# Optimization experiments

Measured on AMD Instinct MI355X. Metric: run time of the kernel, lower is better.

## Reference

```python
import jax, jax.numpy as jnp
import numpy as np

N = 100000   # nodes
E = 1600000  # edges
G = 256      # graphs in batch
IN = 128     # in_feats
H = 64       # h_feats


def _xavier(k, shape):
    fan_in, fan_out = shape
    lim = float(np.sqrt(6.0 / (fan_in + fan_out)))
    return jax.random.uniform(k, shape, jnp.float32, -lim, lim)


def setup_inputs() -> dict:
    key = jax.random.key(0)
    ks = jax.random.split(key, 12)
    x = jax.random.normal(ks[0], (N, IN), jnp.float32)
    src = jax.random.randint(ks[1], (E,), 0, N)
    dst = jax.random.randint(ks[2], (E,), 0, N)
    ew = jax.random.uniform(ks[3], (E,), jnp.float32)
    gid = jnp.sort(jax.random.randint(ks[4], (N,), 0, G))
    def lin(k, fi, fo):
        kw, kb = jax.random.split(k)
        lim = float(np.sqrt(1.0 / fi))
        return (jax.random.uniform(kw, (fi, fo), jnp.float32, -lim, lim),
                jax.random.uniform(kb, (fo,), jnp.float32, -lim, lim))
    W1 = _xavier(ks[5], (IN, H)); b1 = jnp.zeros((H,), jnp.float32)
    W2 = _xavier(ks[6], (H, H));  b2 = jnp.zeros((H,), jnp.float32)
    W3 = _xavier(ks[7], (H, H));  b3 = jnp.zeros((H,), jnp.float32)
    Dw1, Db1 = lin(ks[8], H, 16)
    Dw2, Db2 = lin(ks[9], 16, 8)
    Dw3, Db3 = lin(ks[10], 8, 1)
    return {"x": x, "src": src, "dst": dst, "ew": ew, "gid": gid,
            "W1": W1, "b1": b1, "W2": W2, "b2": b2, "W3": W3, "b3": b3,
            "Dw1": Dw1, "Db1": Db1, "Dw2": Dw2, "Db2": Db2, "Dw3": Dw3, "Db3": Db3}


def reference(x, src, dst, ew, gid, W1, b1, W2, b2, W3, b3,
              Dw1, Db1, Dw2, Db2, Dw3, Db3):
    n = x.shape[0]
    # DGL GraphConv norm='both': unweighted degrees, clamped to >= 1
    deg_out = jnp.zeros((n,), x.dtype).at[src].add(1.0)
    deg_in = jnp.zeros((n,), x.dtype).at[dst].add(1.0)
    ns = jax.lax.rsqrt(jnp.maximum(deg_out, 1.0))  # src-side norm
    nd = jax.lax.rsqrt(jnp.maximum(deg_in, 1.0))   # dst-side norm

    def conv(h, W, b):
        # apply weight first (in >= out), then gather-scale-scatter
        h = (h * ns[:, None]) @ W                      # [N, out]
        m = h[src] * ew[:, None]                       # [E, out] edge messages
        agg = jnp.zeros((n, W.shape[1]), h.dtype).at[dst].add(m)
        return agg * nd[:, None] + b

    h = jax.nn.relu(conv(x, W1, b1))
    h = jax.nn.relu(conv(h, W2, b2))
    h = jax.nn.relu(conv(h, W3, b3))

    # mean_nodes: per-graph mean pooling
    counts = jnp.zeros((G,), h.dtype).at[gid].add(1.0)
    pooled = jnp.zeros((G, h.shape[1]), h.dtype).at[gid].add(h)
    pooled = pooled / jnp.maximum(counts, 1.0)[:, None]

    h = jax.nn.relu(pooled @ Dw1 + Db1)
    h = jax.nn.relu(h @ Dw2 + Db2)
    return jax.nn.sigmoid(h @ Dw3 + Db3)  # [G, 1]
```

## Files before the change

### kernel.cpp

```cpp
#include <hip/hip_runtime.h>
#include <math.h>

#define N_NODES 100000
#define N_EDGES 1600000
#define G_GRAPHS 256
#define IN_F 128
#define H_F 64

#define HB 20
#define HCHUNK (N_EDGES / HB)
#define NWORDS (N_NODES / 4)
#define HNODES 25000
#define HWORDS (HNODES / 4)
#define HR 4

#define NREG 160
#define REG_NODES 625
#define BUCKET_CAP 11000
#define BSPAN 6400
#define NB_BUCKET (N_EDGES / BSPAN)
#define NQ 4
#define QDIV 25000

typedef unsigned int uint_t;
typedef unsigned short ushort_t;
typedef unsigned char uchar_t;
typedef __attribute__((ext_vector_type(8))) short short8;
typedef __attribute__((ext_vector_type(4))) float floatx4;
typedef __attribute__((ext_vector_type(2))) float floatx2;

__device__ __forceinline__ ushort_t f2bf(float f) {
  uint_t u = __float_as_uint(f);
  uint_t r = (u + 0x7fffu + ((u >> 16) & 1u)) >> 16;
  return (ushort_t)r;
}
__device__ __forceinline__ float bflo(uint_t u) { return __uint_as_float(u << 16); }
__device__ __forceinline__ uchar_t f2fp8(float f) {
  return (uchar_t)(__builtin_amdgcn_cvt_pk_fp8_f32(f, f, 0, false) & 0xff);
}
__device__ __forceinline__ int sw_idx(int row, int kshort) {
  int slot = kshort >> 3;
  return row * 64 + (((slot ^ (row & 7)) << 3) | (kshort & 7));
}

__global__ __launch_bounds__(256) void build_a_kernel(
    const int* __restrict__ src, const int* __restrict__ dst,
    const float* __restrict__ ew, int* __restrict__ bcnt,
    uint2* __restrict__ bucket, uint_t* __restrict__ p8src) {
  __shared__ uint_t shm[BSPAN + 2 * NREG];
  if (blockIdx.x < NB_BUCKET) {
    uint_t* rl = shm;
    int* cnt = (int*)(shm + BSPAN);
    int* cur = cnt + NREG;
    const int e0 = blockIdx.x * BSPAN;

    for (int i = threadIdx.x; i < NREG; i += 256) cnt[i] = 0;
    __syncthreads();

    for (int i = threadIdx.x; i < BSPAN; i += 256) {
      uint_t d = (uint_t)dst[e0 + i];
      uint_t r = d / REG_NODES;
      uint_t loc = d - r * REG_NODES;
      rl[i] = (r << 16) | loc;
      atomicAdd(&cnt[r], 1);
    }
    __syncthreads();

    for (int i = threadIdx.x; i < NREG; i += 256)
      cur[i] = atomicAdd(&bcnt[i], cnt[i]);
    __syncthreads();

    for (int i = threadIdx.x; i < BSPAN; i += 256) {
      uint_t v = rl[i];
      uint_t r = v >> 16, loc = v & 0xffffu;
      int pos = atomicAdd(&cur[r], 1);
      if (pos < BUCKET_CAP)
        bucket[(size_t)r * BUCKET_CAP + pos] = make_uint2(
            (loc << 17) | (uint_t)src[e0 + i], __float_as_uint(ew[e0 + i]));
    }
  } else {
    uint_t* h = shm;
    const int idx = blockIdx.x - NB_BUCKET;
    const int r = idx / HB;
    const int b = idx % HB;
    const uint_t rbase = (uint_t)(r * HNODES);

    for (int i = threadIdx.x; i < HWORDS; i += 256) h[i] = 0u;
    __syncthreads();

    const uint4* k4 = (const uint4*)(src + b * HCHUNK);
    for (int i = threadIdx.x; i < HCHUNK / 4; i += 256) {
      uint4 v = k4[i];
      uint_t t;
      t = v.x - rbase; if (t < (uint_t)HNODES) atomicAdd(&h[t >> 2], 1u << ((t & 3u) * 8u));
      t = v.y - rbase; if (t < (uint_t)HNODES) atomicAdd(&h[t >> 2], 1u << ((t & 3u) * 8u));
      t = v.z - rbase; if (t < (uint_t)HNODES) atomicAdd(&h[t >> 2], 1u << ((t & 3u) * 8u));
      t = v.w - rbase; if (t < (uint_t)HNODES) atomicAdd(&h[t >> 2], 1u << ((t & 3u) * 8u));
    }
    __syncthreads();

    uint_t* outp = p8src + (size_t)b * NWORDS + r * HWORDS;
    for (int i = threadIdx.x; i < HWORDS; i += 256) outp[i] = h[i];
  }
}

__global__ __launch_bounds__(1024) void build_b_kernel(
    const uint2* __restrict__ bucket, const int* __restrict__ bcnt,
    const uint_t* __restrict__ p8src, uint_t* __restrict__ csr,
    int2* __restrict__ rc, float* __restrict__ nd, float* __restrict__ ns) {
  __shared__ uint_t staged[BUCKET_CAP];
  __shared__ int cnt4[REG_NODES * NQ];
  __shared__ int sc4[REG_NODES * NQ];
  __shared__ int ts[1024];
  const int tid = threadIdx.x;
  if (blockIdx.x >= NREG) {
    int w = (blockIdx.x - NREG) * 1024 + tid;
    if (w >= NWORDS) return;
    int c0 = 0, c1 = 0, c2 = 0, c3 = 0;
    for (int b = 0; b < HB; ++b) {
      uint_t xv = p8src[(size_t)b * NWORDS + w];
      c0 += (int)(xv & 0xffu);
      c1 += (int)((xv >> 8) & 0xffu);
      c2 += (int)((xv >> 16) & 0xffu);
      c3 += (int)((xv >> 24) & 0xffu);
    }
    ((float4*)ns)[w] = make_float4(
        rsqrtf(fmaxf((float)c0, 1.0f)), rsqrtf(fmaxf((float)c1, 1.0f)),
        rsqrtf(fmaxf((float)c2, 1.0f)), rsqrtf(fmaxf((float)c3, 1.0f)));
    return;
  }
  const int r = blockIdx.x;
  const int nE = min(bcnt[r], BUCKET_CAP);

  ts[tid] = (tid < NREG) ? min(bcnt[tid], BUCKET_CAP) : 0;
  for (int i = tid; i < REG_NODES * NQ; i += 1024) cnt4[i] = 0;
  __syncthreads();
  for (int off = 1; off < 256; off <<= 1) {
    int t = (tid >= off) ? ts[tid - off] : 0;
    __syncthreads();
    ts[tid] += t;
    __syncthreads();
  }
  const int csr_base = (r == 0) ? 0 : ts[r - 1];
  __syncthreads();

  const uint2* bk = bucket + (size_t)r * BUCKET_CAP;
  for (int i = tid; i < nE; i += 1024) {
    uint_t ex = bk[i].x;
    uint_t loc = ex >> 17;
    uint_t q = (ex & 0x1ffffu) / QDIV;
    atomicAdd(&cnt4[loc * NQ + q], 1);
  }
  __syncthreads();

  int c4[NQ], cv = 0;
  if (tid < REG_NODES) {
#pragma unroll
    for (int q = 0; q < NQ; ++q) { c4[q] = cnt4[tid * NQ + q]; cv += c4[q]; }
  }
  ts[tid] = (tid < REG_NODES) ? cv : 0;
  __syncthreads();
  for (int off = 1; off < 1024; off <<= 1) {
    int t = (tid >= off) ? ts[tid - off] : 0;
    __syncthreads();
    ts[tid] += t;
    __syncthreads();
  }
  if (tid < REG_NODES) {
    int run = (tid == 0) ? 0 : ts[tid - 1];
    int v = r * REG_NODES + tid;
    rc[v] = make_int2(csr_base + run, cv);
    nd[v] = rsqrtf(fmaxf((float)cv, 1.0f));
#pragma unroll
    for (int q = 0; q < NQ; ++q) { sc4[tid * NQ + q] = run; run += c4[q]; }
  }
  __syncthreads();

  for (int i = tid; i < nE; i += 1024) {
    uint2 e = bk[i];
    uint_t loc = e.x >> 17;
    uint_t q = (e.x & 0x1ffffu) / QDIV;
    int pos = atomicAdd(&sc4[loc * NQ + q], 1);
    staged[pos] = ((uint_t)(f2bf(__uint_as_float(e.y)) & 0x7fff) << 17) |
                  (e.x & 0x1ffffu);
  }
  __syncthreads();

  for (int i = tid; i < nE; i += 1024) csr[csr_base + i] = staged[i];
}

template <int K, bool AFP32>
__global__ __launch_bounds__(256) void gemm_mfma_kernel(
    const void* __restrict__ Xin, const float* __restrict__ W,
    const float* __restrict__ ns, uchar_t* __restrict__ T, int ntiles) {
  constexpr int CH = K / 32;
  constexpr int WROW = K + 8;
  __shared__ __align__(16) ushort_t Wt[64 * WROW];
  const int tid = threadIdx.x;

  for (int i = tid; i < K * 64; i += 256) {
    int k = i >> 6, nn = i & 63;
    Wt[nn * WROW + k] = f2bf(W[i]);
  }
  __syncthreads();

  const int wave = tid >> 6;
  const int lane = tid & 63;
  const int tile = blockIdx.x * 4 + wave;
  if (tile >= ntiles) return;
  const int m = lane & 15;
  const int q = lane >> 4;
  const int node0 = tile * 16;

  short8 afrag[CH];
  if (AFP32) {
    const float* xr = (const float*)Xin + (size_t)(node0 + m) * K + q * 8;
#pragma unroll
    for (int c = 0; c < CH; ++c) {
      float4 xa = *(const float4*)(xr + c * 32);
      float4 xb = *(const float4*)(xr + c * 32 + 4);
      short8 a;
      a[0] = (short)f2bf(xa.x); a[1] = (short)f2bf(xa.y);
      a[2] = (short)f2bf(xa.z); a[3] = (short)f2bf(xa.w);
      a[4] = (short)f2bf(xb.x); a[5] = (short)f2bf(xb.y);
      a[6] = (short)f2bf(xb.z); a[7] = (short)f2bf(xb.w);
      afrag[c] = a;
    }
  } else {
    const ushort_t* xr = (const ushort_t*)Xin + (size_t)(node0 + m) * K + q * 8;
#pragma unroll
    for (int c = 0; c < CH; ++c)
      afrag[c] = *(const short8*)(xr + c * 32);
  }

  floatx4 acc[4];
#pragma unroll
  for (int t = 0; t < 4; ++t) acc[t] = (floatx4){0.f, 0.f, 0.f, 0.f};

#pragma unroll
  for (int t = 0; t < 4; ++t) {
    const ushort_t* wr = &Wt[(t * 16 + m) * WROW + q * 8];
#pragma unroll
    for (int c = 0; c < CH; ++c) {
      short8 bfrag = *(const short8*)(wr + c * 32);
      acc[t] = __builtin_amdgcn_mfma_f32_16x16x32_bf16(afrag[c], bfrag, acc[t], 0, 0, 0);
    }
  }

  float4 nsv = *(const float4*)(ns + node0 + q * 4);
  const float nsa[4] = {nsv.x, nsv.y, nsv.z, nsv.w};
#pragma unroll
  for (int t = 0; t < 4; ++t) {
#pragma unroll
    for (int r = 0; r < 4; ++r) {
      int node = node0 + q * 4 + r;
      T[(size_t)node * 64 + t * 16 + m] = f2fp8(acc[t][r] * nsa[r]);
    }
  }
}

__device__ __forceinline__ void gacc1(float acc[8], uint_t e, uint2 p) {
  float w = __uint_as_float((e >> 17) << 16);
  floatx2 a;
  a = __builtin_amdgcn_cvt_pk_f32_fp8(p.x, false);
  acc[0] = fmaf(a.x, w, acc[0]); acc[1] = fmaf(a.y, w, acc[1]);
  a = __builtin_amdgcn_cvt_pk_f32_fp8(p.x, true);
  acc[2] = fmaf(a.x, w, acc[2]); acc[3] = fmaf(a.y, w, acc[3]);
  a = __builtin_amdgcn_cvt_pk_f32_fp8(p.y, false);
  acc[4] = fmaf(a.x, w, acc[4]); acc[5] = fmaf(a.y, w, acc[5]);
  a = __builtin_amdgcn_cvt_pk_f32_fp8(p.y, true);
  acc[6] = fmaf(a.x, w, acc[6]); acc[7] = fmaf(a.y, w, acc[7]);
}

template <bool POOL>
__global__ __launch_bounds__(256, 6) void fused_kernel(
    const uint_t* __restrict__ csr, const int2* __restrict__ rc,
    const uchar_t* __restrict__ T, const float* __restrict__ nd,
    const float* __restrict__ bias, const float* __restrict__ ns,
    const float* __restrict__ W, uchar_t* __restrict__ Tout,
    const int* __restrict__ gid, float* __restrict__ pooled) {
  __shared__ __align__(16) ushort_t Hs[POOL ? 8 : 64 * 64];
  __shared__ __align__(16) ushort_t Wt[POOL ? 8 : 64 * 64];
  __shared__ float gaccF[POOL ? 256 : 1];
  __shared__ int g0s;
  const int tid = threadIdx.x;
  const int node_base = blockIdx.x * 64;
  const int vlast = min(node_base + 63, N_NODES - 1);

  if constexpr (POOL) {
    gaccF[tid] = 0.0f;
    if (tid == 0) g0s = gid[node_base];
  } else {
    for (int i = tid; i < H_F * 64; i += 256) {
      int k = i >> 6, nn = i & 63;
      Wt[sw_idx(nn, k)] = f2bf(W[i]);
    }
  }
  __syncthreads();

  const int lane = tid & 63;
  const int wv = tid >> 6;
  const int o = lane >> 3, l = lane & 7;
  const uint2* Tp = (const uint2*)T;

  const float4 b0 = *(const float4*)&bias[l * 8];
  const float4 b1v = *(const float4*)&bias[l * 8 + 4];

#pragma unroll 1
  for (int pass = 0; pass < 2; ++pass) {
    const int ln = pass * 32 + wv * 8 + o;
    const int v = node_base + ln;
    if (v < N_NODES) {
      int2 rcv = rc[v];
      int k = rcv.x;
      const int ke = rcv.x + rcv.y;
      float acc[8] = {0, 0, 0, 0, 0, 0, 0, 0};

      for (; k + 4 <= ke; k += 4) {
        uint_t e0 = csr[k], e1 = csr[k + 1], e2 = csr[k + 2], e3 = csr[k + 3];
        uint2 p0 = Tp[(size_t)(e0 & 0x1ffffu) * 8 + l];
        uint2 p1 = Tp[(size_t)(e1 & 0x1ffffu) * 8 + l];
        uint2 p2 = Tp[(size_t)(e2 & 0x1ffffu) * 8 + l];
        uint2 p3 = Tp[(size_t)(e3 & 0x1ffffu) * 8 + l];
        gacc1(acc, e0, p0); gacc1(acc, e1, p1);
        gacc1(acc, e2, p2); gacc1(acc, e3, p3);
      }
      for (; k < ke; ++k) {
        uint_t e0 = csr[k];
        uint2 p0 = Tp[(size_t)(e0 & 0x1ffffu) * 8 + l];
        gacc1(acc, e0, p0);
      }

      const float ndv = nd[v];
      if constexpr (!POOL) {
        uint4 ov;
        ov.x = (uint_t)f2bf(fmaxf(fmaf(acc[0], ndv, b0.x), 0.f)) |
               ((uint_t)f2bf(fmaxf(fmaf(acc[1], ndv, b0.y), 0.f)) << 16);
        ov.y = (uint_t)f2bf(fmaxf(fmaf(acc[2], ndv, b0.z), 0.f)) |
               ((uint_t)f2bf(fmaxf(fmaf(acc[3], ndv, b0.w), 0.f)) << 16);
        ov.z = (uint_t)f2bf(fmaxf(fmaf(acc[4], ndv, b1v.x), 0.f)) |
               ((uint_t)f2bf(fmaxf(fmaf(acc[5], ndv, b1v.y), 0.f)) << 16);
        ov.w = (uint_t)f2bf(fmaxf(fmaf(acc[6], ndv, b1v.z), 0.f)) |
               ((uint_t)f2bf(fmaxf(fmaf(acc[7], ndv, b1v.w), 0.f)) << 16);
        *((uint4*)&Hs[sw_idx(ln, l * 8)]) = ov;
      } else {
        const float bb[8] = {b0.x, b0.y, b0.z, b0.w, b1v.x, b1v.y, b1v.z, b1v.w};
        float vals[8];
#pragma unroll
        for (int f = 0; f < 8; ++f)
          vals[f] = bflo((uint_t)f2bf(fmaxf(fmaf(acc[f], ndv, bb[f]), 0.f)));
        int g = gid[v];
        int gl = g - g0s;
        if (gl >= 0 && gl < 4) {
#pragma unroll
          for (int f = 0; f < 8; ++f)
            atomicAdd(&gaccF[gl * 64 + l * 8 + f], vals[f]);
        } else {
#pragma unroll
          for (int f = 0; f < 8; ++f)
            atomicAdd(&pooled[(size_t)g * 64 + l * 8 + f], vals[f]);
        }
      }
    }
  }
  __syncthreads();

  if constexpr (!POOL) {
    const int m = lane & 15, q = lane >> 4;
    const int node0 = node_base + wv * 16;
    if (node0 < N_NODES) {
      short8 afrag[2];
      afrag[0] = *(const short8*)&Hs[sw_idx(wv * 16 + m, q * 8)];
      afrag[1] = *(const short8*)&Hs[sw_idx(wv * 16 + m, q * 8 + 32)];

      floatx4 acc4v[4];
#pragma unroll
      for (int t = 0; t < 4; ++t) acc4v[t] = (floatx4){0.f, 0.f, 0.f, 0.f};
#pragma unroll
      for (int t = 0; t < 4; ++t) {
#pragma unroll
        for (int c = 0; c < 2; ++c) {
          short8 bfrag = *(const short8*)&Wt[sw_idx(t * 16 + m, q * 8 + c * 32)];
          acc4v[t] = __builtin_amdgcn_mfma_f32_16x16x32_bf16(afrag[c], bfrag,
                                                            acc4v[t], 0, 0, 0);
        }
      }
      float4 nsv = *(const float4*)(ns + node0 + q * 4);
      const float nsa[4] = {nsv.x, nsv.y, nsv.z, nsv.w};
#pragma unroll
      for (int t = 0; t < 4; ++t) {
#pragma unroll
        for (int r2 = 0; r2 < 4; ++r2) {
          int node = node0 + q * 4 + r2;
          Tout[(size_t)node * 64 + t * 16 + m] = f2fp8(acc4v[t][r2] * nsa[r2]);
        }
      }
    }
  } else {
    int span = gid[vlast] - g0s + 1;
    if (span > 4) span = 4;
    if (tid < span * 64) {
      int gl = tid >> 6, j = tid & 63;
      int g = g0s + gl;
      if (g < G_GRAPHS) {
        float vsum = gaccF[gl * 64 + j];
        if (vsum != 0.0f) atomicAdd(&pooled[(size_t)g * 64 + j], vsum);
      }
    }
  }
}

__global__ __launch_bounds__(256) void pool_mlp_kernel(
    const float* __restrict__ pooled, const int* __restrict__ gid,
    const float* __restrict__ Dw1, const float* __restrict__ Db1,
    const float* __restrict__ Dw2, const float* __restrict__ Db2,
    const float* __restrict__ Dw3, const float* __restrict__ Db3,
    float* __restrict__ out) {
  __shared__ float mean[64];
  __shared__ float h1s[16], h2s[8];
  const int g = blockIdx.x;
  int l = 0, r = N_NODES;
  while (l < r) { int m = (l + r) >> 1; if (gid[m] < g) l = m + 1; else r = m; }
  const int lo = l;
  r = N_NODES;
  while (l < r) { int m = (l + r) >> 1; if (gid[m] < g + 1) l = m + 1; else r = m; }
  const int hi = l;

  if (threadIdx.x < 64) {
    float inv = 1.0f / fmaxf((float)(hi - lo), 1.0f);
    mean[threadIdx.x] = pooled[(size_t)g * 64 + threadIdx.x] * inv;
  }
  __syncthreads();
  if (threadIdx.x < 16) {
    int o = threadIdx.x;
    float a = Db1[o];
#pragma unroll
    for (int k = 0; k < 64; ++k) a = fmaf(mean[k], Dw1[k * 16 + o], a);
    h1s[o] = fmaxf(a, 0.0f);
  }
  __syncthreads();
  if (threadIdx.x < 8) {
    int o = threadIdx.x;
    float a = Db2[o];
#pragma unroll
    for (int k = 0; k < 16; ++k) a = fmaf(h1s[k], Dw2[k * 8 + o], a);
    h2s[o] = fmaxf(a, 0.0f);
  }
  __syncthreads();
  if (threadIdx.x == 0) {
    float a = Db3[0];
#pragma unroll
    for (int k = 0; k < 8; ++k) a = fmaf(h2s[k], Dw3[k], a);
    out[g] = 1.0f / (1.0f + expf(-a));
  }
}

extern "C" void kernel_launch(void* const* d_in, const int* in_sizes, int n_in,
                              void* d_out, int out_size, void* d_ws, size_t ws_size,
                              hipStream_t stream) {
  const float* x   = (const float*)d_in[0];
  const int*   src = (const int*)  d_in[1];
  const int*   dst = (const int*)  d_in[2];
  const float* ew  = (const float*)d_in[3];
  const int*   gid = (const int*)  d_in[4];
  const float* W1  = (const float*)d_in[5];
  const float* b1  = (const float*)d_in[6];
  const float* W2  = (const float*)d_in[7];
  const float* b2  = (const float*)d_in[8];
  const float* W3  = (const float*)d_in[9];
  const float* b3  = (const float*)d_in[10];
  const float* Dw1 = (const float*)d_in[11];
  const float* Db1 = (const float*)d_in[12];
  const float* Dw2 = (const float*)d_in[13];
  const float* Db2 = (const float*)d_in[14];
  const float* Dw3 = (const float*)d_in[15];
  const float* Db3 = (const float*)d_in[16];
  float* out = (float*)d_out;

  char* ws = (char*)d_ws;
  const size_t TSZ = (size_t)N_NODES * 64;
  const size_t BUCKET_BYTES = (size_t)NREG * BUCKET_CAP * 8;
  uchar_t*  T_a   = (uchar_t*)ws;
  uchar_t*  T_b   = (uchar_t*)(ws + TSZ);
  uint2*    bucket = (uint2*)ws;
  char* p = ws + BUCKET_BYTES;
  uint_t*   csr   = (uint_t*)p;          p += (size_t)N_EDGES * 4;
  uint_t*   p8src = (uint_t*)p;          p += (size_t)HB * NWORDS * 4;
  float*    ns    = (float*)p;           p += (size_t)N_NODES * 4;
  float*    nd    = (float*)p;           p += (size_t)N_NODES * 4;
  int2*     rc    = (int2*)p;            p += (size_t)N_NODES * 8;
  int*      bcnt  = (int*)p;             p += (size_t)NREG * 4;
  float*    pooled = (float*)p;

  const int NTILES  = N_NODES / 16;
  const int NB_A    = NB_BUCKET + HR * HB;
  const int NB_B    = NREG + (NWORDS + 1023) / 1024;
  const int NB_GEMM = (NTILES + 3) / 4;
  const int NB_F    = (N_NODES + 63) / 64;

  hipMemsetAsync(bcnt, 0,
                 NREG * sizeof(int) + G_GRAPHS * H_F * sizeof(float), stream);
  build_a_kernel<<<NB_A, 256, 0, stream>>>(src, dst, ew, bcnt, bucket, p8src);
  build_b_kernel<<<NB_B, 1024, 0, stream>>>(bucket, bcnt, p8src, csr, rc, nd, ns);

  gemm_mfma_kernel<IN_F, true><<<NB_GEMM, 256, 0, stream>>>(x, W1, ns, T_a, NTILES);
  fused_kernel<false><<<NB_F, 256, 0, stream>>>(csr, rc, T_a, nd, b1, ns, W2,
                                                T_b, nullptr, nullptr);
  fused_kernel<false><<<NB_F, 256, 0, stream>>>(csr, rc, T_b, nd, b2, ns, W3,
                                                T_a, nullptr, nullptr);
  fused_kernel<true><<<NB_F, 256, 0, stream>>>(csr, rc, T_a, nd, b3, nullptr,
                                               nullptr, nullptr, gid, pooled);

  pool_mlp_kernel<<<G_GRAPHS, 256, 0, stream>>>(pooled, gid, Dw1, Db1, Dw2, Db2,
                                                Dw3, Db3, out);
}
```

Measured before the change: 314.4 us.

## Gather 16 fp8 features per lane and drop source-quadrant CSR sorting

The aggregation kernel now assigns 4 lanes per node, each loading a uint4 (16 fp8 features), so a wavefront covers 16 nodes in a single pass instead of 8 nodes per pass over two passes. This makes the gathers wider and gives more edges in flight per wave, at the cost of more accumulator registers per thread. The CSR build step also stops sub-sorting each destination's edges by source quadrant, which removes the per-edge division and the 4x larger shared count arrays. That sorting may have been providing gather locality that is now lost.

```diff
diff --git a/kernel.cpp b/kernel.cpp
--- a/kernel.cpp
+++ b/kernel.cpp
@@ -19,8 +19,6 @@
 #define BUCKET_CAP 11000
 #define BSPAN 6400
 #define NB_BUCKET (N_EDGES / BSPAN)
-#define NQ 4
-#define QDIV 25000
 
 typedef unsigned int uint_t;
 typedef unsigned short ushort_t;
@@ -109,8 +107,8 @@
     const uint_t* __restrict__ p8src, uint_t* __restrict__ csr,
     int2* __restrict__ rc, float* __restrict__ nd, float* __restrict__ ns) {
   __shared__ uint_t staged[BUCKET_CAP];
-  __shared__ int cnt4[REG_NODES * NQ];
-  __shared__ int sc4[REG_NODES * NQ];
+  __shared__ int cnt[REG_NODES];
+  __shared__ int sc[REG_NODES];
   __shared__ int ts[1024];
   const int tid = threadIdx.x;
   if (blockIdx.x >= NREG) {
@@ -133,7 +131,7 @@
   const int nE = min(bcnt[r], BUCKET_CAP);
 
   ts[tid] = (tid < NREG) ? min(bcnt[tid], BUCKET_CAP) : 0;
-  for (int i = tid; i < REG_NODES * NQ; i += 1024) cnt4[i] = 0;
+  for (int i = tid; i < REG_NODES; i += 1024) cnt[i] = 0;
   __syncthreads();
   for (int off = 1; off < 256; off <<= 1) {
     int t = (tid >= off) ? ts[tid - off] : 0;
@@ -145,20 +143,11 @@
   __syncthreads();
 
   const uint2* bk = bucket + (size_t)r * BUCKET_CAP;
-  for (int i = tid; i < nE; i += 1024) {
-    uint_t ex = bk[i].x;
-    uint_t loc = ex >> 17;
-    uint_t q = (ex & 0x1ffffu) / QDIV;
-    atomicAdd(&cnt4[loc * NQ + q], 1);
-  }
-  __syncthreads();
-
-  int c4[NQ], cv = 0;
-  if (tid < REG_NODES) {
-#pragma unroll
-    for (int q = 0; q < NQ; ++q) { c4[q] = cnt4[tid * NQ + q]; cv += c4[q]; }
-  }
-  ts[tid] = (tid < REG_NODES) ? cv : 0;
+  for (int i = tid; i < nE; i += 1024) atomicAdd(&cnt[bk[i].x >> 17], 1);
+  __syncthreads();
+
+  int cv = (tid < REG_NODES) ? cnt[tid] : 0;
+  ts[tid] = cv;
   __syncthreads();
   for (int off = 1; off < 1024; off <<= 1) {
     int t = (tid >= off) ? ts[tid - off] : 0;
@@ -168,19 +157,17 @@
   }
   if (tid < REG_NODES) {
     int run = (tid == 0) ? 0 : ts[tid - 1];
+    sc[tid] = run;
     int v = r * REG_NODES + tid;
     rc[v] = make_int2(csr_base + run, cv);
     nd[v] = rsqrtf(fmaxf((float)cv, 1.0f));
-#pragma unroll
-    for (int q = 0; q < NQ; ++q) { sc4[tid * NQ + q] = run; run += c4[q]; }
   }
   __syncthreads();
 
   for (int i = tid; i < nE; i += 1024) {
     uint2 e = bk[i];
     uint_t loc = e.x >> 17;
-    uint_t q = (e.x & 0x1ffffu) / QDIV;
-    int pos = atomicAdd(&sc4[loc * NQ + q], 1);
+    int pos = atomicAdd(&sc[loc], 1);
     staged[pos] = ((uint_t)(f2bf(__uint_as_float(e.y)) & 0x7fff) << 17) |
                   (e.x & 0x1ffffu);
   }
@@ -259,17 +246,19 @@
   }
 }
 
-__device__ __forceinline__ void gacc1(float acc[8], uint_t e, uint2 p) {
-  float w = __uint_as_float((e >> 17) << 16);
+__device__ __forceinline__ void gaccq(float acc[16], uint_t e, uint4 p) {
+  const float w = __uint_as_float((e >> 17) << 16);
+  const uint_t pu[4] = {p.x, p.y, p.z, p.w};
   floatx2 a;
-  a = __builtin_amdgcn_cvt_pk_f32_fp8(p.x, false);
-  acc[0] = fmaf(a.x, w, acc[0]); acc[1] = fmaf(a.y, w, acc[1]);
-  a = __builtin_amdgcn_cvt_pk_f32_fp8(p.x, true);
-  acc[2] = fmaf(a.x, w, acc[2]); acc[3] = fmaf(a.y, w, acc[3]);
-  a = __builtin_amdgcn_cvt_pk_f32_fp8(p.y, false);
-  acc[4] = fmaf(a.x, w, acc[4]); acc[5] = fmaf(a.y, w, acc[5]);
-  a = __builtin_amdgcn_cvt_pk_f32_fp8(p.y, true);
-  acc[6] = fmaf(a.x, w, acc[6]); acc[7] = fmaf(a.y, w, acc[7]);
+#pragma unroll
+  for (int u = 0; u < 4; ++u) {
+    a = __builtin_amdgcn_cvt_pk_f32_fp8(pu[u], false);
+    acc[u * 4 + 0] = fmaf(a.x, w, acc[u * 4 + 0]);
+    acc[u * 4 + 1] = fmaf(a.y, w, acc[u * 4 + 1]);
+    a = __builtin_amdgcn_cvt_pk_f32_fp8(pu[u], true);
+    acc[u * 4 + 2] = fmaf(a.x, w, acc[u * 4 + 2]);
+    acc[u * 4 + 3] = fmaf(a.y, w, acc[u * 4 + 3]);
+  }
 }
 
 template <bool POOL>
@@ -300,66 +289,74 @@
 
   const int lane = tid & 63;
   const int wv = tid >> 6;
-  const int o = lane >> 3, l = lane & 7;
-  const uint2* Tp = (const uint2*)T;
-
-  const float4 b0 = *(const float4*)&bias[l * 8];
-  const float4 b1v = *(const float4*)&bias[l * 8 + 4];
-
-#pragma unroll 1
-  for (int pass = 0; pass < 2; ++pass) {
-    const int ln = pass * 32 + wv * 8 + o;
-    const int v = node_base + ln;
-    if (v < N_NODES) {
-      int2 rcv = rc[v];
-      int k = rcv.x;
-      const int ke = rcv.x + rcv.y;
-      float acc[8] = {0, 0, 0, 0, 0, 0, 0, 0};
-
-      for (; k + 4 <= ke; k += 4) {
-        uint_t e0 = csr[k], e1 = csr[k + 1], e2 = csr[k + 2], e3 = csr[k + 3];
-        uint2 p0 = Tp[(size_t)(e0 & 0x1ffffu) * 8 + l];
-        uint2 p1 = Tp[(size_t)(e1 & 0x1ffffu) * 8 + l];
-        uint2 p2 = Tp[(size_t)(e2 & 0x1ffffu) * 8 + l];
-        uint2 p3 = Tp[(size_t)(e3 & 0x1ffffu) * 8 + l];
-        gacc1(acc, e0, p0); gacc1(acc, e1, p1);
-        gacc1(acc, e2, p2); gacc1(acc, e3, p3);
-      }
-      for (; k < ke; ++k) {
-        uint_t e0 = csr[k];
-        uint2 p0 = Tp[(size_t)(e0 & 0x1ffffu) * 8 + l];
-        gacc1(acc, e0, p0);
-      }
-
-      const float ndv = nd[v];
-      if constexpr (!POOL) {
-        uint4 ov;
-        ov.x = (uint_t)f2bf(fmaxf(fmaf(acc[0], ndv, b0.x), 0.f)) |
-               ((uint_t)f2bf(fmaxf(fmaf(acc[1], ndv, b0.y), 0.f)) << 16);
-        ov.y = (uint_t)f2bf(fmaxf(fmaf(acc[2], ndv, b0.z), 0.f)) |
-               ((uint_t)f2bf(fmaxf(fmaf(acc[3], ndv, b0.w), 0.f)) << 16);
-        ov.z = (uint_t)f2bf(fmaxf(fmaf(acc[4], ndv, b1v.x), 0.f)) |
-               ((uint_t)f2bf(fmaxf(fmaf(acc[5], ndv, b1v.y), 0.f)) << 16);
-        ov.w = (uint_t)f2bf(fmaxf(fmaf(acc[6], ndv, b1v.z), 0.f)) |
-               ((uint_t)f2bf(fmaxf(fmaf(acc[7], ndv, b1v.w), 0.f)) << 16);
-        *((uint4*)&Hs[sw_idx(ln, l * 8)]) = ov;
+  const int qd = lane >> 2;
+  const int l = lane & 3;
+  const int row = wv * 16 + qd;
+  const int v = node_base + row;
+  const uint4* Tq = (const uint4*)T;
+
+  float acc[16];
+#pragma unroll
+  for (int f = 0; f < 16; ++f) acc[f] = 0.0f;
+
+  if (v < N_NODES) {
+    int2 rcv = rc[v];
+    int k = rcv.x;
+    const int ke = rcv.x + rcv.y;
+    for (; k + 4 <= ke; k += 4) {
+      uint_t e0 = csr[k], e1 = csr[k + 1], e2 = csr[k + 2], e3 = csr[k + 3];
+      uint4 p0 = Tq[(size_t)(e0 & 0x1ffffu) * 4 + l];
+      uint4 p1 = Tq[(size_t)(e1 & 0x1ffffu) * 4 + l];
+      uint4 p2 = Tq[(size_t)(e2 & 0x1ffffu) * 4 + l];
+      uint4 p3 = Tq[(size_t)(e3 & 0x1ffffu) * 4 + l];
+      gaccq(acc, e0, p0); gaccq(acc, e1, p1);
+      gaccq(acc, e2, p2); gaccq(acc, e3, p3);
+    }
+    for (; k < ke; ++k) {
+      uint_t e0 = csr[k];
+      uint4 p0 = Tq[(size_t)(e0 & 0x1ffffu) * 4 + l];
+      gaccq(acc, e0, p0);
+    }
+  }
+
+  if (v < N_NODES) {
+    const float ndv = nd[v];
+    const float4 ba = *(const float4*)&bias[l * 16];
+    const float4 bb = *(const float4*)&bias[l * 16 + 4];
+    const float4 bc = *(const float4*)&bias[l * 16 + 8];
+    const float4 bd = *(const float4*)&bias[l * 16 + 12];
+    const float bl[16] = {ba.x, ba.y, ba.z, ba.w, bb.x, bb.y, bb.z, bb.w,
+                          bc.x, bc.y, bc.z, bc.w, bd.x, bd.y, bd.z, bd.w};
+    float vals[16];
+#pragma unroll
+    for (int f = 0; f < 16; ++f)
+      vals[f] = fmaxf(fmaf(acc[f], ndv, bl[f]), 0.0f);
+
+    if constexpr (!POOL) {
+      uint4 ov0, ov1;
+      ov0.x = (uint_t)f2bf(vals[0]) | ((uint_t)f2bf(vals[1]) << 16);
+      ov0.y = (uint_t)f2bf(vals[2]) | ((uint_t)f2bf(vals[3]) << 16);
+      ov0.z = (uint_t)f2bf(vals[4]) | ((uint_t)f2bf(vals[5]) << 16);
+      ov0.w = (uint_t)f2bf(vals[6]) | ((uint_t)f2bf(vals[7]) << 16);
+      ov1.x = (uint_t)f2bf(vals[8]) | ((uint_t)f2bf(vals[9]) << 16);
+      ov1.y = (uint_t)f2bf(vals[10]) | ((uint_t)f2bf(vals[11]) << 16);
+      ov1.z = (uint_t)f2bf(vals[12]) | ((uint_t)f2bf(vals[13]) << 16);
+      ov1.w = (uint_t)f2bf(vals[14]) | ((uint_t)f2bf(vals[15]) << 16);
+      *((uint4*)&Hs[sw_idx(row, l * 16)]) = ov0;
+      *((uint4*)&Hs[sw_idx(row, l * 16 + 8)]) = ov1;
+    } else {
+      const int g = gid[v];
+      const int gl = g - g0s;
+      if (gl >= 0 && gl < 4) {
+#pragma unroll
+        for (int f = 0; f < 16; ++f)
+          atomicAdd(&gaccF[gl * 64 + l * 16 + f],
+                    bflo((uint_t)f2bf(vals[f])));
       } else {
-        const float bb[8] = {b0.x, b0.y, b0.z, b0.w, b1v.x, b1v.y, b1v.z, b1v.w};
-        float vals[8];
-#pragma unroll
-        for (int f = 0; f < 8; ++f)
-          vals[f] = bflo((uint_t)f2bf(fmaxf(fmaf(acc[f], ndv, bb[f]), 0.f)));
-        int g = gid[v];
-        int gl = g - g0s;
-        if (gl >= 0 && gl < 4) {
-#pragma unroll
-          for (int f = 0; f < 8; ++f)
-            atomicAdd(&gaccF[gl * 64 + l * 8 + f], vals[f]);
-        } else {
-#pragma unroll
-          for (int f = 0; f < 8; ++f)
-            atomicAdd(&pooled[(size_t)g * 64 + l * 8 + f], vals[f]);
-        }
+#pragma unroll
+        for (int f = 0; f < 16; ++f)
+          atomicAdd(&pooled[(size_t)g * 64 + l * 16 + f],
+                    bflo((uint_t)f2bf(vals[f])));
       }
     }
   }
```

After: 292.8 us. 6.8% less time.

## Fuse CSR build with first-layer GEMM and drop per-node source sub-bucketing

Applied to the files above, without the earlier changes.

Merges the CSR build kernel and the layer-1 MFMA GEMM into one launch. CSR-building blocks run beside GEMM blocks that compute the source-degree norm locally and keep it in shared memory. The per-node quartile sub-sort (NQ=4, with a division per edge) is removed, so edges inside a destination node are no longer ordered by source, which may hurt gather locality later. The workspace is re-laid out so T buffers no longer alias the bucket region, which lets the GEMM write T while buckets are still being read. One kernel launch and the serialization between the two phases go away.

```diff
diff --git a/kernel.cpp b/kernel.cpp
--- a/kernel.cpp
+++ b/kernel.cpp
@@ -19,8 +19,9 @@
 #define BUCKET_CAP 11000
 #define BSPAN 6400
 #define NB_BUCKET (N_EDGES / BSPAN)
-#define NQ 4
-#define QDIV 25000
+
+#define NTILES_C 6250
+#define NB_GEMMW 391
 
 typedef unsigned int uint_t;
 typedef unsigned short ushort_t;
@@ -104,119 +105,55 @@
   }
 }
 
-__global__ __launch_bounds__(1024) void build_b_kernel(
+__global__ __launch_bounds__(1024, 2) void buildb_gemm_kernel(
     const uint2* __restrict__ bucket, const int* __restrict__ bcnt,
-    const uint_t* __restrict__ p8src, uint_t* __restrict__ csr,
-    int2* __restrict__ rc, float* __restrict__ nd, float* __restrict__ ns) {
-  __shared__ uint_t staged[BUCKET_CAP];
-  __shared__ int cnt4[REG_NODES * NQ];
-  __shared__ int sc4[REG_NODES * NQ];
-  __shared__ int ts[1024];
+    const uint_t* __restrict__ p8src, const float* __restrict__ x,
+    const float* __restrict__ W1, uint_t* __restrict__ csr,
+    int2* __restrict__ rc, float* __restrict__ nd, float* __restrict__ ns,
+    uchar_t* __restrict__ T) {
+  __shared__ __align__(16) char shm_u[53104];
   const int tid = threadIdx.x;
+
   if (blockIdx.x >= NREG) {
-    int w = (blockIdx.x - NREG) * 1024 + tid;
-    if (w >= NWORDS) return;
-    int c0 = 0, c1 = 0, c2 = 0, c3 = 0;
-    for (int b = 0; b < HB; ++b) {
-      uint_t xv = p8src[(size_t)b * NWORDS + w];
-      c0 += (int)(xv & 0xffu);
-      c1 += (int)((xv >> 8) & 0xffu);
-      c2 += (int)((xv >> 16) & 0xffu);
-      c3 += (int)((xv >> 24) & 0xffu);
-    }
-    ((float4*)ns)[w] = make_float4(
-        rsqrtf(fmaxf((float)c0, 1.0f)), rsqrtf(fmaxf((float)c1, 1.0f)),
-        rsqrtf(fmaxf((float)c2, 1.0f)), rsqrtf(fmaxf((float)c3, 1.0f)));
-    return;
-  }
-  const int r = blockIdx.x;
-  const int nE = min(bcnt[r], BUCKET_CAP);
-
-  ts[tid] = (tid < NREG) ? min(bcnt[tid], BUCKET_CAP) : 0;
-  for (int i = tid; i < REG_NODES * NQ; i += 1024) cnt4[i] = 0;
-  __syncthreads();
-  for (int off = 1; off < 256; off <<= 1) {
-    int t = (tid >= off) ? ts[tid - off] : 0;
-    __syncthreads();
-    ts[tid] += t;
-    __syncthreads();
-  }
-  const int csr_base = (r == 0) ? 0 : ts[r - 1];
-  __syncthreads();
-
-  const uint2* bk = bucket + (size_t)r * BUCKET_CAP;
-  for (int i = tid; i < nE; i += 1024) {
-    uint_t ex = bk[i].x;
-    uint_t loc = ex >> 17;
-    uint_t q = (ex & 0x1ffffu) / QDIV;
-    atomicAdd(&cnt4[loc * NQ + q], 1);
-  }
-  __syncthreads();
-
-  int c4[NQ], cv = 0;
-  if (tid < REG_NODES) {
-#pragma unroll
-    for (int q = 0; q < NQ; ++q) { c4[q] = cnt4[tid * NQ + q]; cv += c4[q]; }
-  }
-  ts[tid] = (tid < REG_NODES) ? cv : 0;
-  __syncthreads();
-  for (int off = 1; off < 1024; off <<= 1) {
-    int t = (tid >= off) ? ts[tid - off] : 0;
-    __syncthreads();
-    ts[tid] += t;
-    __syncthreads();
-  }
-  if (tid < REG_NODES) {
-    int run = (tid == 0) ? 0 : ts[tid - 1];
-    int v = r * REG_NODES + tid;
-    rc[v] = make_int2(csr_base + run, cv);
-    nd[v] = rsqrtf(fmaxf((float)cv, 1.0f));
-#pragma unroll
-    for (int q = 0; q < NQ; ++q) { sc4[tid * NQ + q] = run; run += c4[q]; }
-  }
-  __syncthreads();
-
-  for (int i = tid; i < nE; i += 1024) {
-    uint2 e = bk[i];
-    uint_t loc = e.x >> 17;
-    uint_t q = (e.x & 0x1ffffu) / QDIV;
-    int pos = atomicAdd(&sc4[loc * NQ + q], 1);
-    staged[pos] = ((uint_t)(f2bf(__uint_as_float(e.y)) & 0x7fff) << 17) |
-                  (e.x & 0x1ffffu);
-  }
-  __syncthreads();
-
-  for (int i = tid; i < nE; i += 1024) csr[csr_base + i] = staged[i];
-}
-
-template <int K, bool AFP32>
-__global__ __launch_bounds__(256) void gemm_mfma_kernel(
-    const void* __restrict__ Xin, const float* __restrict__ W,
-    const float* __restrict__ ns, uchar_t* __restrict__ T, int ntiles) {
-  constexpr int CH = K / 32;
-  constexpr int WROW = K + 8;
-  __shared__ __align__(16) ushort_t Wt[64 * WROW];
-  const int tid = threadIdx.x;
-
-  for (int i = tid; i < K * 64; i += 256) {
-    int k = i >> 6, nn = i & 63;
-    Wt[nn * WROW + k] = f2bf(W[i]);
-  }
-  __syncthreads();
-
-  const int wave = tid >> 6;
-  const int lane = tid & 63;
-  const int tile = blockIdx.x * 4 + wave;
-  if (tile >= ntiles) return;
-  const int m = lane & 15;
-  const int q = lane >> 4;
-  const int node0 = tile * 16;
-
-  short8 afrag[CH];
-  if (AFP32) {
-    const float* xr = (const float*)Xin + (size_t)(node0 + m) * K + q * 8;
-#pragma unroll
-    for (int c = 0; c < CH; ++c) {
+    constexpr int WROW = IN_F + 8;
+    ushort_t* Wt = (ushort_t*)shm_u;
+    float* ns_s = (float*)(shm_u + 17408);
+
+    for (int i = tid; i < IN_F * 64; i += 1024) {
+      int k = i >> 6, nn = i & 63;
+      Wt[nn * WROW + k] = f2bf(W1[i]);
+    }
+    __syncthreads();
+
+    const int wv = tid >> 6;
+    const int lane = tid & 63;
+    const int tile = (blockIdx.x - NREG) * 16 + wv;
+    if (tile >= NTILES_C) return;
+    const int node0 = tile * 16;
+    const int m = lane & 15;
+    const int q = lane >> 4;
+
+    if (lane < 4) {
+      const int w = tile * 4 + lane;
+      int c0 = 0, c1 = 0, c2 = 0, c3 = 0;
+      for (int b = 0; b < HB; ++b) {
+        uint_t xv = p8src[(size_t)b * NWORDS + w];
+        c0 += (int)(xv & 0xffu);
+        c1 += (int)((xv >> 8) & 0xffu);
+        c2 += (int)((xv >> 16) & 0xffu);
+        c3 += (int)((xv >> 24) & 0xffu);
+      }
+      float4 nv = make_float4(
+          rsqrtf(fmaxf((float)c0, 1.0f)), rsqrtf(fmaxf((float)c1, 1.0f)),
+          rsqrtf(fmaxf((float)c2, 1.0f)), rsqrtf(fmaxf((float)c3, 1.0f)));
+      ((float4*)ns)[w] = nv;
+      *(float4*)&ns_s[wv * 16 + lane * 4] = nv;
+    }
+
+    short8 afrag[4];
+    const float* xr = x + (size_t)(node0 + m) * IN_F + q * 8;
+#pragma unroll
+    for (int c = 0; c < 4; ++c) {
       float4 xa = *(const float4*)(xr + c * 32);
       float4 xb = *(const float4*)(xr + c * 32 + 4);
       short8 a;
@@ -226,37 +163,83 @@
       a[6] = (short)f2bf(xb.z); a[7] = (short)f2bf(xb.w);
       afrag[c] = a;
     }
-  } else {
-    const ushort_t* xr = (const ushort_t*)Xin + (size_t)(node0 + m) * K + q * 8;
-#pragma unroll
-    for (int c = 0; c < CH; ++c)
-      afrag[c] = *(const short8*)(xr + c * 32);
-  }
-
-  floatx4 acc[4];
-#pragma unroll
-  for (int t = 0; t < 4; ++t) acc[t] = (floatx4){0.f, 0.f, 0.f, 0.f};
-
-#pragma unroll
-  for (int t = 0; t < 4; ++t) {
-    const ushort_t* wr = &Wt[(t * 16 + m) * WROW + q * 8];
-#pragma unroll
-    for (int c = 0; c < CH; ++c) {
-      short8 bfrag = *(const short8*)(wr + c * 32);
-      acc[t] = __builtin_amdgcn_mfma_f32_16x16x32_bf16(afrag[c], bfrag, acc[t], 0, 0, 0);
-    }
-  }
-
-  float4 nsv = *(const float4*)(ns + node0 + q * 4);
-  const float nsa[4] = {nsv.x, nsv.y, nsv.z, nsv.w};
-#pragma unroll
-  for (int t = 0; t < 4; ++t) {
-#pragma unroll
-    for (int r = 0; r < 4; ++r) {
-      int node = node0 + q * 4 + r;
-      T[(size_t)node * 64 + t * 16 + m] = f2fp8(acc[t][r] * nsa[r]);
-    }
-  }
+
+    floatx4 acc[4];
+#pragma unroll
+    for (int t = 0; t < 4; ++t) acc[t] = (floatx4){0.f, 0.f, 0.f, 0.f};
+#pragma unroll
+    for (int t = 0; t < 4; ++t) {
+      const ushort_t* wr = &Wt[(t * 16 + m) * WROW + q * 8];
+#pragma unroll
+      for (int c = 0; c < 4; ++c) {
+        short8 bfrag = *(const short8*)(wr + c * 32);
+        acc[t] = __builtin_amdgcn_mfma_f32_16x16x32_bf16(afrag[c], bfrag,
+                                                         acc[t], 0, 0, 0);
+      }
+    }
+#pragma unroll
+    for (int t = 0; t < 4; ++t) {
+#pragma unroll
+      for (int r = 0; r < 4; ++r) {
+        int node = node0 + q * 4 + r;
+        T[(size_t)node * 64 + t * 16 + m] =
+            f2fp8(acc[t][r] * ns_s[wv * 16 + q * 4 + r]);
+      }
+    }
+    return;
+  }
+
+  uint_t* staged = (uint_t*)shm_u;
+  int* cnt = (int*)(shm_u + 44000);
+  int* sc = (int*)(shm_u + 46500);
+  int* ts = (int*)(shm_u + 49000);
+  const int r = blockIdx.x;
+  const int nE = min(bcnt[r], BUCKET_CAP);
+
+  ts[tid] = (tid < NREG) ? min(bcnt[tid], BUCKET_CAP) : 0;
+  for (int i = tid; i < REG_NODES; i += 1024) cnt[i] = 0;
+  __syncthreads();
+  for (int off = 1; off < 256; off <<= 1) {
+    int t = (tid >= off) ? ts[tid - off] : 0;
+    __syncthreads();
+    ts[tid] += t;
+    __syncthreads();
+  }
+  const int csr_base = (r == 0) ? 0 : ts[r - 1];
+  __syncthreads();
+
+  const uint2* bk = bucket + (size_t)r * BUCKET_CAP;
+  for (int i = tid; i < nE; i += 1024) atomicAdd(&cnt[bk[i].x >> 17], 1);
+  __syncthreads();
+
+  int cv = (tid < REG_NODES) ? cnt[tid] : 0;
+  ts[tid] = cv;
+  __syncthreads();
+  for (int off = 1; off < 1024; off <<= 1) {
+    int t = (tid >= off) ? ts[tid - off] : 0;
+    __syncthreads();
+    ts[tid] += t;
+    __syncthreads();
+  }
+  if (tid < REG_NODES) {
+    int run = (tid == 0) ? 0 : ts[tid - 1];
+    sc[tid] = run;
+    int v = r * REG_NODES + tid;
+    rc[v] = make_int2(csr_base + run, cv);
+    nd[v] = rsqrtf(fmaxf((float)cv, 1.0f));
+  }
+  __syncthreads();
+
+  for (int i = tid; i < nE; i += 1024) {
+    uint2 e = bk[i];
+    uint_t loc = e.x >> 17;
+    int pos = atomicAdd(&sc[loc], 1);
+    staged[pos] = ((uint_t)(f2bf(__uint_as_float(e.y)) & 0x7fff) << 17) |
+                  (e.x & 0x1ffffu);
+  }
+  __syncthreads();
+
+  for (int i = tid; i < nE; i += 1024) csr[csr_base + i] = staged[i];
 }
 
 __device__ __forceinline__ void gacc1(float acc[8], uint_t e, uint2 p) {
@@ -477,40 +460,33 @@
   const float* Db3 = (const float*)d_in[16];
   float* out = (float*)d_out;
 
-  char* ws = (char*)d_ws;
-  const size_t TSZ = (size_t)N_NODES * 64;
-  const size_t BUCKET_BYTES = (size_t)NREG * BUCKET_CAP * 8;
-  uchar_t*  T_a   = (uchar_t*)ws;
-  uchar_t*  T_b   = (uchar_t*)(ws + TSZ);
-  uint2*    bucket = (uint2*)ws;
-  char* p = ws + BUCKET_BYTES;
+  char* p = (char*)d_ws;
+  uint2*    bucket = (uint2*)p;          p += (size_t)NREG * BUCKET_CAP * 8;
   uint_t*   csr   = (uint_t*)p;          p += (size_t)N_EDGES * 4;
   uint_t*   p8src = (uint_t*)p;          p += (size_t)HB * NWORDS * 4;
   float*    ns    = (float*)p;           p += (size_t)N_NODES * 4;
   float*    nd    = (float*)p;           p += (size_t)N_NODES * 4;
   int2*     rc    = (int2*)p;            p += (size_t)N_NODES * 8;
   int*      bcnt  = (int*)p;             p += (size_t)NREG * 4;
-  float*    pooled = (float*)p;
-
-  const int NTILES  = N_NODES / 16;
-  const int NB_A    = NB_BUCKET + HR * HB;
-  const int NB_B    = NREG + (NWORDS + 1023) / 1024;
-  const int NB_GEMM = (NTILES + 3) / 4;
-  const int NB_F    = (N_NODES + 63) / 64;
+  float*    pooled = (float*)p;          p += (size_t)G_GRAPHS * H_F * 4;
+  uchar_t*  T_a   = (uchar_t*)p;         p += (size_t)N_NODES * 64;
+  uchar_t*  T_b   = (uchar_t*)p;
+
+  const int NB_A = NB_BUCKET + HR * HB;
+  const int NB_M = NREG + NB_GEMMW;
+  const int NB_F = (N_NODES + 63) / 64;
 
   hipMemsetAsync(bcnt, 0,
                  NREG * sizeof(int) + G_GRAPHS * H_F * sizeof(float), stream);
   build_a_kernel<<<NB_A, 256, 0, stream>>>(src, dst, ew, bcnt, bucket, p8src);
-  build_b_kernel<<<NB_B, 1024, 0, stream>>>(bucket, bcnt, p8src, csr, rc, nd, ns);
-
-  gemm_mfma_kernel<IN_F, true><<<NB_GEMM, 256, 0, stream>>>(x, W1, ns, T_a, NTILES);
+  buildb_gemm_kernel<<<NB_M, 1024, 0, stream>>>(bucket, bcnt, p8src, x, W1,
+                                                csr, rc, nd, ns, T_a);
   fused_kernel<false><<<NB_F, 256, 0, stream>>>(csr, rc, T_a, nd, b1, ns, W2,
                                                 T_b, nullptr, nullptr);
   fused_kernel<false><<<NB_F, 256, 0, stream>>>(csr, rc, T_b, nd, b2, ns, W3,
                                                 T_a, nullptr, nullptr);
   fused_kernel<true><<<NB_F, 256, 0, stream>>>(csr, rc, T_a, nd, b3, nullptr,
                                                nullptr, nullptr, gid, pooled);
-
   pool_mlp_kernel<<<G_GRAPHS, 256, 0, stream>>>(pooled, gid, Dw1, Db1, Dw2, Db2,
                                                 Dw3, Db3, out);
 }
```

Result: faster. 306.8 us (-2.4%).
